# Performance work log

Measured on AMD Instinct MI355X. Metric: run time of the kernel, lower is better.

## Reference

```python
import jax, jax.numpy as jnp
import numpy as np

EPS = 1e-12


def _l2norm(x, axis):
    return x / jnp.maximum(jnp.linalg.norm(x, axis=axis, keepdims=True), EPS)


def _wn_weight(v, g):
    # weight norm over input axis (kernel_size=1): W = g * v / ||v||
    return g * v / jnp.maximum(jnp.linalg.norm(v, axis=0, keepdims=True), EPS)


def setup_inputs() -> dict:
    key = jax.random.key(0)
    ks = jax.random.split(key, 8)
    B, T, D = 16, 4096, 512
    N, K, d = 9, 1024, 8
    return {
        "z": jax.random.normal(ks[0], (B, T, D), dtype=jnp.float32),
        "in_v": jax.random.normal(ks[1], (N, D, d), dtype=jnp.float32) * 0.05,
        "in_g": jax.random.uniform(ks[2], (N, d), dtype=jnp.float32) + 0.5,
        "in_b": jax.random.normal(ks[3], (N, d), dtype=jnp.float32) * 0.01,
        "out_v": jax.random.normal(ks[4], (N, d, D), dtype=jnp.float32) * 0.05,
        "out_g": jax.random.uniform(ks[5], (N, D), dtype=jnp.float32) + 0.5,
        "out_b": jax.random.normal(ks[6], (N, D), dtype=jnp.float32) * 0.01,
        "codebooks": jax.random.normal(ks[7], (N, K, d), dtype=jnp.float32),
    }


def reference(z, in_v, in_g, in_b, out_v, out_g, out_b, codebooks):
    # Eval-mode ResidualVectorQuantize: n_quantizers = n_codebooks, mask all True.
    n_codebooks = codebooks.shape[0]
    residual = z
    z_q = jnp.zeros_like(z)
    commitment_loss = jnp.zeros((), z.dtype)
    codebook_loss = jnp.zeros((), z.dtype)
    codes, latents = [], []
    for i in range(n_codebooks):
        # in_proj (weight-normalized 1x1 conv == linear): [B,T,D] -> [B,T,d]
        W_in = _wn_weight(in_v[i], in_g[i])
        z_e = jnp.einsum("btd,dc->btc", residual, W_in) + in_b[i]
        # decode_latents: l2-normalize, pairwise sq-dist, nearest neighbor
        cb = codebooks[i]                      # [K, d] raw codebook
        enc_n = _l2norm(z_e, axis=-1)          # [B, T, d]
        cb_n = _l2norm(cb, axis=-1)            # [K, d]
        dist = (jnp.sum(enc_n * enc_n, -1, keepdims=True)
                - 2.0 * jnp.einsum("btc,kc->btk", enc_n, cb_n)
                + jnp.sum(cb_n * cb_n, -1))    # [B, T, K]
        indices = jnp.argmax(-dist, axis=-1)   # [B, T]
        z_q_i = cb[indices]                    # gather from raw codebook [B,T,d]
        # per-batch losses (mean over T, d)
        commit_i = jnp.mean((z_e - jax.lax.stop_gradient(z_q_i)) ** 2, axis=(1, 2))
        cbloss_i = jnp.mean((z_q_i - jax.lax.stop_gradient(z_e)) ** 2, axis=(1, 2))
        # straight-through estimator
        z_q_st = z_e + jax.lax.stop_gradient(z_q_i - z_e)
        # out_proj: [B,T,d] -> [B,T,D]
        W_out = _wn_weight(out_v[i], out_g[i])
        z_q_proj = jnp.einsum("btc,cd->btd", z_q_st, W_out) + out_b[i]
        z_q = z_q + z_q_proj
        residual = residual - z_q_proj
        commitment_loss = commitment_loss + commit_i.mean()
        codebook_loss = codebook_loss + cbloss_i.mean()
        codes.append(indices)
        latents.append(z_e)
    codes = jnp.stack(codes, axis=2)           # [B, T, N]
    latents = jnp.concatenate(latents, axis=2) # [B, T, N*d]
    return z_q, codes, latents, commitment_loss, codebook_loss
```

## Files before the change

### kernel.cpp

```cpp
#include <hip/hip_runtime.h>
#include <math.h>

#define ROWS   65536

#define WS_WPAD 0
#define WS_WOUT 49152
#define WS_CBT  86016
#define WS_SC   159744
#define WS_M    168960
#define WS_CACC 174144
#define WS_SOB  174216
#define WS_LOSS 174728

#define OUT_CODES 33554432
#define OUT_LAT   34144256
#define OUT_CLOSS 38862848
#define OUT_CBLOSS 38862849

__device__ __forceinline__ int pcol(int cc){ return (cc/9)*12 + (cc%9); }

__global__ __launch_bounds__(256) void prep1(const float* __restrict__ in_v,
    const float* __restrict__ in_g, const float* __restrict__ out_v,
    const float* __restrict__ out_g, const float* __restrict__ out_b,
    const float* __restrict__ cb, float* __restrict__ ws)
{
    int t = blockIdx.x*256 + threadIdx.x;
    if (t < 9216) {
        int i = t >> 10, k = t & 1023;
        const float* p = cb + (i*1024 + k)*8;
        float v[8]; float ssq = 0.f;
        #pragma unroll
        for (int c=0;c<8;c++){ v[c]=p[c]; ssq = fmaf(v[c],v[c],ssq); }
        float den = fmaxf(sqrtf(ssq), 1e-12f);
        float sc = 0.f;
        #pragma unroll
        for (int c=0;c<8;c++){ float cn = v[c]/den; ws[WS_CBT + (i*8+c)*1024 + k] = cn; sc = fmaf(cn,cn,sc); }
        ws[WS_SC + i*1024 + k] = sc;
    } else if (t < 13824) {
        int r = t - 9216; int j = r >> 9, tt = r & 511;
        float v[8]; float ssq = 0.f;
        #pragma unroll
        for (int a=0;a<8;a++){ v[a]=out_v[(j*8+a)*512+tt]; ssq=fmaf(v[a],v[a],ssq); }
        float den = fmaxf(sqrtf(ssq), 1e-12f);
        float g = out_g[j*512+tt];
        #pragma unroll
        for (int a=0;a<8;a++) ws[WS_WOUT + (j*8+a)*512 + tt] = g*v[a]/den;
    } else if (t < 18432) {
        int r = t - 13824;
        int w = r >> 6, l = r & 63;
        int i = w >> 3, c = w & 7;
        float v[8]; float ssq = 0.f;
        #pragma unroll
        for (int u=0;u<8;u++){ v[u] = in_v[(i*512 + l*8+u)*8 + c]; ssq = fmaf(v[u],v[u],ssq); }
        #pragma unroll
        for (int off=1; off<64; off<<=1) ssq += __shfl_xor(ssq, off, 64);
        float den = fmaxf(sqrtf(ssq), 1e-12f);
        float g = in_g[i*8+c];
        int pc = pcol(i*8+c);
        #pragma unroll
        for (int u=0;u<8;u++) ws[WS_WPAD + (l*8+u)*96 + pc] = g*v[u]/den;
    } else if (t < 18944) {
        int tt = t - 18432;
        float s = 0.f;
        for (int j=0;j<9;j++) s += out_b[j*512+tt];
        ws[WS_SOB + tt] = s;
    } else if (t == 18944) {
        *(double*)&ws[WS_LOSS] = 0.0;
    }
}

__global__ __launch_bounds__(256) void prep2(const float* __restrict__ out_b,
                                             float* __restrict__ ws)
{
    int g = blockIdx.x*256 + threadIdx.x;
    if (g < 41472) {
        int oi = g >> 3, part = g & 7;
        int j = oi / 576; int rem = oi % 576; int i = rem >> 6; int ab = rem & 63;
        int a = ab >> 3, b = ab & 7;
        int pc = pcol(i*8+b);
        const float* wo = ws + WS_WOUT + (j*8+a)*512 + part*64;
        const float* wp = ws + WS_WPAD + (part*64)*96 + pc;
        float s = 0.f;
        #pragma unroll
        for (int u=0; u<16; u++) {
            float4 w4 = *(const float4*)(wo + u*4);
            s = fmaf(w4.x, wp[(u*4+0)*96], s);
            s = fmaf(w4.y, wp[(u*4+1)*96], s);
            s = fmaf(w4.z, wp[(u*4+2)*96], s);
            s = fmaf(w4.w, wp[(u*4+3)*96], s);
        }
        #pragma unroll
        for (int off=1; off<8; off<<=1) s += __shfl_xor(s, off, 64);
        if (part == 0) ws[WS_M + oi] = s;
    } else if (g < 42048) {
        int r = g - 41472;
        int oi = r >> 3, part = r & 7;
        int i = oi >> 3, b = oi & 7;
        int pc = pcol(i*8+b);
        float s = 0.f;
        for (int u=0; u<64; u++) {
            int tt = part*64 + u;
            float bb = 0.f;
            for (int j=0;j<i;j++) bb += out_b[j*512+tt];
            s = fmaf(bb, ws[WS_WPAD + tt*96+pc], s);
        }
        #pragma unroll
        for (int off=1; off<8; off<<=1) s += __shfl_xor(s, off, 64);
        if (part == 0) ws[WS_CACC + oi] = s;
    }
}

__global__ __launch_bounds__(256) void gemm_in(const float* __restrict__ z,
    const float* __restrict__ in_b, const float* __restrict__ ws, float* __restrict__ out)
{
    __shared__ float AsT[32*132];
    __shared__ float Bs[32*96];
    int tid = threadIdx.x;
    int rowbase = blockIdx.x * 128;
    int tr = tid & 31, tc = tid >> 5;
    float acc[4][9];
    #pragma unroll
    for (int r=0;r<4;r++){
        #pragma unroll
        for(int c=0;c<9;c++) acc[r][c]=0.f;
    }
    int kq = tid & 7, rr = tid >> 3;
    for (int kk=0; kk<16; kk++) {
        #pragma unroll
        for (int p=0;p<4;p++){
            int row = rr + p*32;
            float4 a = *(const float4*)(z + (size_t)(rowbase+row)*512 + kk*32 + kq*4);
            AsT[(kq*4+0)*132 + row] = a.x;
            AsT[(kq*4+1)*132 + row] = a.y;
            AsT[(kq*4+2)*132 + row] = a.z;
            AsT[(kq*4+3)*132 + row] = a.w;
        }
        #pragma unroll
        for (int p=0;p<3;p++){
            int idx = p*256 + tid;
            *(float4*)(Bs + idx*4) = *(const float4*)(ws + WS_WPAD + kk*32*96 + idx*4);
        }
        __syncthreads();
        #pragma unroll 4
        for (int k=0;k<32;k++){
            float4 a  = *(const float4*)(AsT + k*132 + tr*4);
            float4 b0 = *(const float4*)(Bs + k*96 + tc*12);
            float4 b1 = *(const float4*)(Bs + k*96 + tc*12 + 4);
            float  b8 = Bs[k*96 + tc*12 + 8];
            float av[4] = {a.x,a.y,a.z,a.w};
            float bv[9] = {b0.x,b0.y,b0.z,b0.w,b1.x,b1.y,b1.z,b1.w,b8};
            #pragma unroll
            for (int r=0;r<4;r++){
                #pragma unroll
                for (int c=0;c<9;c++) acc[r][c] = fmaf(av[r], bv[c], acc[r][c]);
            }
        }
        __syncthreads();
    }
    #pragma unroll
    for (int c=0;c<9;c++){
        int cc = tc*9+c;
        float bias = in_b[cc];
        #pragma unroll
        for (int r=0;r<4;r++){
            int row = rowbase + tr*4 + r;
            out[OUT_LAT + (size_t)row*72 + cc] = acc[r][c] + bias;
        }
    }
}

__global__ __launch_bounds__(256) void step_all(
    const float* __restrict__ cbooks, float* __restrict__ ws, float* __restrict__ out)
{
    __shared__ float lds_cb[8*1056];
    __shared__ float lds_sc[8*132];
    __shared__ float codes_lds[128*13];
    __shared__ float warr[4];

    int tid = threadIdx.x;
    int oct = tid & 7;
    int rowslot = tid >> 3;
    int rowbase = blockIdx.x * 128;
    const int kbase = oct*128;
    const float* cbo = lds_cb + oct*132;
    const float* sco = lds_sc + oct*132;

    float lacc = 0.f;

    for (int i=0; i<9; i++){
        __syncthreads();
        #pragma unroll
        for (int p=0;p<8;p++){
            int s = (p*256 + tid)*4;
            int c = s >> 10; int k = s & 1023; int o = k >> 7; int kk = k & 127;
            float4 v = *(const float4*)(ws + WS_CBT + i*8192 + s);
            *(float4*)(lds_cb + c*1056 + o*132 + kk) = v;
        }
        {
            int s = tid*4;
            int o = s >> 7; int kk = s & 127;
            float4 v = *(const float4*)(ws + WS_SC + i*1024 + s);
            v.x *= 0.5f; v.y *= 0.5f; v.z *= 0.5f; v.w *= 0.5f;
            *(float4*)(lds_sc + o*132 + kk) = v;
        }
        __syncthreads();

        float zen[4][8];
        #pragma unroll
        for (int r=0;r<4;r++){
            int rib = r*32 + rowslot;
            int row = rowbase + rib;
            float* lat = out + OUT_LAT + (size_t)row*72 + i*8;
            float4 p0 = *(const float4*)(lat);
            float4 p1 = *(const float4*)(lat+4);
            float ze[8] = {p0.x,p0.y,p0.z,p0.w,p1.x,p1.y,p1.z,p1.w};
            #pragma unroll
            for (int b=0;b<8;b++) ze[b] -= ws[WS_CACC + i*8 + b];
            for (int j=0;j<i;j++){
                int kj = (int)codes_lds[rib*13 + j];
                const float* qp = cbooks + (size_t)(j*1024+kj)*8;
                float4 q0 = *(const float4*)(qp);
                float4 q1 = *(const float4*)(qp+4);
                float qa[8] = {q0.x,q0.y,q0.z,q0.w,q1.x,q1.y,q1.z,q1.w};
                const float* M = ws + WS_M + (j*9+i)*64;
                #pragma unroll
                for (int a=0;a<8;a++){
                    #pragma unroll
                    for (int b=0;b<8;b++) ze[b] = fmaf(-qa[a], M[a*8+b], ze[b]);
                }
            }
            float ssq = 0.f;
            #pragma unroll
            for (int c=0;c<8;c++) ssq = fmaf(ze[c],ze[c],ssq);
            float den = fmaxf(sqrtf(ssq), 1e-12f);
            float rden = 1.0f/den;
            if (oct == 0){
                float4 z0 = {ze[0],ze[1],ze[2],ze[3]};
                float4 z1 = {ze[4],ze[5],ze[6],ze[7]};
                *(float4*)(lat)   = z0;
                *(float4*)(lat+4) = z1;
            }
            #pragma unroll
            for (int c=0;c<8;c++) zen[r][c] = ze[c]*rden;
        }

        float bv[4]; int bk[4];
        #pragma unroll
        for (int r=0;r<4;r++){ bv[r] = -3.0e38f; bk[r] = kbase; }
        #pragma unroll 2
        for (int kk=0; kk<128; kk+=4){
            float4 v[8];
            #pragma unroll
            for (int c=0;c<8;c++) v[c] = *(const float4*)(cbo + c*1056 + kk);
            float4 hs = *(const float4*)(sco + kk);
            #pragma unroll
            for (int r=0;r<4;r++){
                float d0=0.f,d1=0.f,d2=0.f,d3=0.f;
                #pragma unroll
                for (int c=0;c<8;c++){
                    d0 = fmaf(zen[r][c], v[c].x, d0);
                    d1 = fmaf(zen[r][c], v[c].y, d1);
                    d2 = fmaf(zen[r][c], v[c].z, d2);
                    d3 = fmaf(zen[r][c], v[c].w, d3);
                }
                float t0 = d0 - hs.x;
                float t1 = d1 - hs.y;
                float t2 = d2 - hs.z;
                float t3 = d3 - hs.w;
                bool c0 = t0 > bv[r]; bk[r] = c0?(kbase+kk+0):bk[r]; bv[r] = c0?t0:bv[r];
                bool c1 = t1 > bv[r]; bk[r] = c1?(kbase+kk+1):bk[r]; bv[r] = c1?t1:bv[r];
                bool c2 = t2 > bv[r]; bk[r] = c2?(kbase+kk+2):bk[r]; bv[r] = c2?t2:bv[r];
                bool c3 = t3 > bv[r]; bk[r] = c3?(kbase+kk+3):bk[r]; bv[r] = c3?t3:bv[r];
            }
        }

        #pragma unroll
        for (int off=1; off<8; off<<=1){
            #pragma unroll
            for (int r=0;r<4;r++){
                float ov = __shfl_xor(bv[r], off, 64);
                int   ok = __shfl_xor(bk[r], off, 64);
                bool rep = (ov > bv[r]) || (ov == bv[r] && ok < bk[r]);
                bv[r] = rep ? ov : bv[r];
                bk[r] = rep ? ok : bk[r];
            }
        }
        if (oct == 0){
            #pragma unroll
            for (int r=0;r<4;r++){
                int rib = r*32 + rowslot;
                int row = rowbase + rib;
                out[OUT_CODES + (size_t)row*9 + i] = (float)bk[r];
                codes_lds[rib*13 + i] = (float)bk[r];
                const float* lat = out + OUT_LAT + (size_t)row*72 + i*8;
                const float* qp = cbooks + (size_t)(i*1024+bk[r])*8;
                float4 z0 = *(const float4*)(lat);
                float4 z1 = *(const float4*)(lat+4);
                float4 q0 = *(const float4*)(qp);
                float4 q1 = *(const float4*)(qp+4);
                float e0 = z0.x-q0.x, e1 = z0.y-q0.y, e2 = z0.z-q0.z, e3 = z0.w-q0.w;
                float e4 = z1.x-q1.x, e5 = z1.y-q1.y, e6 = z1.z-q1.z, e7 = z1.w-q1.w;
                lacc = fmaf(e0,e0,lacc); lacc = fmaf(e1,e1,lacc);
                lacc = fmaf(e2,e2,lacc); lacc = fmaf(e3,e3,lacc);
                lacc = fmaf(e4,e4,lacc); lacc = fmaf(e5,e5,lacc);
                lacc = fmaf(e6,e6,lacc); lacc = fmaf(e7,e7,lacc);
            }
        }
    }

    #pragma unroll
    for (int off=1; off<64; off<<=1) lacc += __shfl_xor(lacc, off, 64);
    if ((tid & 63)==0) warr[tid>>6] = lacc;
    __syncthreads();
    if (tid==0){
        double bs = (double)warr[0]+(double)warr[1]+(double)warr[2]+(double)warr[3];
        atomicAdd((double*)&ws[WS_LOSS], bs);
    }
}

__global__ __launch_bounds__(256) void gemm_out(const float* __restrict__ cbooks,
    const float* __restrict__ ws, float* __restrict__ out)
{
    __shared__ float QL[64*76];
    __shared__ float Ws[72*128];
    int tid = threadIdx.x;
    int rowbase = blockIdx.x*64;
    if (tid < 64){
        int row = rowbase + tid;
        for (int j=0;j<9;j++){
            int kj = (int)out[OUT_CODES + (size_t)row*9 + j];
            const float* qp = cbooks + (j*1024+kj)*8;
            float4 q0 = *(const float4*)qp;
            float4 q1 = *(const float4*)(qp+4);
            *(float4*)(QL + tid*76 + j*8)     = q0;
            *(float4*)(QL + tid*76 + j*8 + 4) = q1;
        }
    }
    int tr = tid & 15, tc = tid >> 4;
    for (int cc=0; cc<4; cc++){
        __syncthreads();
        #pragma unroll
        for (int p=0;p<9;p++){
            int idx = p*256 + tid;
            int jr = idx >> 5; int cq = idx & 31;
            *(float4*)(Ws + jr*128 + cq*4) = *(const float4*)(ws + WS_WOUT + jr*512 + cc*128 + cq*4);
        }
        __syncthreads();
        float acc[4][8];
        #pragma unroll
        for (int r=0;r<4;r++){
            #pragma unroll
            for (int c=0;c<8;c++) acc[r][c]=0.f;
        }
        #pragma unroll 4
        for (int k=0;k<72;k++){
            float a0 = QL[(tr*4+0)*76 + k];
            float a1 = QL[(tr*4+1)*76 + k];
            float a2 = QL[(tr*4+2)*76 + k];
            float a3 = QL[(tr*4+3)*76 + k];
            float4 b0 = *(const float4*)(Ws + k*128 + tc*8);
            float4 b1 = *(const float4*)(Ws + k*128 + tc*8 + 4);
            float bv[8] = {b0.x,b0.y,b0.z,b0.w,b1.x,b1.y,b1.z,b1.w};
            float av[4] = {a0,a1,a2,a3};
            #pragma unroll
            for (int r=0;r<4;r++){
                #pragma unroll
                for (int c=0;c<8;c++) acc[r][c] = fmaf(av[r], bv[c], acc[r][c]);
            }
        }
        float4 s0 = *(const float4*)(ws + WS_SOB + cc*128 + tc*8);
        float4 s1 = *(const float4*)(ws + WS_SOB + cc*128 + tc*8 + 4);
        #pragma unroll
        for (int r=0;r<4;r++){
            int row = rowbase + tr*4 + r;
            float4 o0 = {acc[r][0]+s0.x, acc[r][1]+s0.y, acc[r][2]+s0.z, acc[r][3]+s0.w};
            float4 o1 = {acc[r][4]+s1.x, acc[r][5]+s1.y, acc[r][6]+s1.z, acc[r][7]+s1.w};
            *(float4*)(out + (size_t)row*512 + cc*128 + tc*8)     = o0;
            *(float4*)(out + (size_t)row*512 + cc*128 + tc*8 + 4) = o1;
        }
    }
    if (blockIdx.x==0 && tid==0){
        double L = *(const double*)(ws + WS_LOSS);
        float lv = (float)(L * (1.0/524288.0));
        out[OUT_CLOSS]  = lv;
        out[OUT_CBLOSS] = lv;
    }
}

extern "C" void kernel_launch(void* const* d_in, const int* in_sizes, int n_in,
                              void* d_out, int out_size, void* d_ws, size_t ws_size,
                              hipStream_t stream) {
    const float* z     = (const float*)d_in[0];
    const float* in_v  = (const float*)d_in[1];
    const float* in_g  = (const float*)d_in[2];
    const float* in_b  = (const float*)d_in[3];
    const float* out_v = (const float*)d_in[4];
    const float* out_g = (const float*)d_in[5];
    const float* out_b = (const float*)d_in[6];
    const float* cb    = (const float*)d_in[7];
    float* out = (float*)d_out;
    float* ws  = (float*)d_ws;

    prep1<<<75, 256, 0, stream>>>(in_v, in_g, out_v, out_g, out_b, cb, ws);
    prep2<<<165, 256, 0, stream>>>(out_b, ws);
    gemm_in<<<512, 256, 0, stream>>>(z, in_b, ws, out);
    step_all<<<512, 256, 0, stream>>>(cb, ws, out);
    gemm_out<<<1024, 256, 0, stream>>>(cb, ws, out);
}
```

Measured before the change: 660.4 us.

## Widen step_all to 512 threads and retile gemm_out to 8x8 transposed tiles

Measured after the change: 677.2 us. 2.5% more time.

```diff
diff --git a/kernel.cpp b/kernel.cpp
--- a/kernel.cpp
+++ b/kernel.cpp
@@ -169,13 +169,13 @@
     }
 }
 
-__global__ __launch_bounds__(256) void step_all(
+__global__ __launch_bounds__(512, 4) void step_all(
     const float* __restrict__ cbooks, float* __restrict__ ws, float* __restrict__ out)
 {
     __shared__ float lds_cb[8*1056];
     __shared__ float lds_sc[8*132];
     __shared__ float codes_lds[128*13];
-    __shared__ float warr[4];
+    __shared__ float warr[8];
 
     int tid = threadIdx.x;
     int oct = tid & 7;
@@ -190,13 +190,13 @@
     for (int i=0; i<9; i++){
         __syncthreads();
         #pragma unroll
-        for (int p=0;p<8;p++){
-            int s = (p*256 + tid)*4;
+        for (int p=0;p<4;p++){
+            int s = (p*512 + tid)*4;
             int c = s >> 10; int k = s & 1023; int o = k >> 7; int kk = k & 127;
             float4 v = *(const float4*)(ws + WS_CBT + i*8192 + s);
             *(float4*)(lds_cb + c*1056 + o*132 + kk) = v;
         }
-        {
+        if (tid < 256){
             int s = tid*4;
             int o = s >> 7; int kk = s & 127;
             float4 v = *(const float4*)(ws + WS_SC + i*1024 + s);
@@ -205,10 +205,10 @@
         }
         __syncthreads();
 
-        float zen[4][8];
-        #pragma unroll
-        for (int r=0;r<4;r++){
-            int rib = r*32 + rowslot;
+        float zen[2][8];
+        #pragma unroll
+        for (int r=0;r<2;r++){
+            int rib = r*64 + rowslot;
             int row = rowbase + rib;
             float* lat = out + OUT_LAT + (size_t)row*72 + i*8;
             float4 p0 = *(const float4*)(lat);
@@ -244,9 +244,9 @@
             for (int c=0;c<8;c++) zen[r][c] = ze[c]*rden;
         }
 
-        float bv[4]; int bk[4];
-        #pragma unroll
-        for (int r=0;r<4;r++){ bv[r] = -3.0e38f; bk[r] = kbase; }
+        float bv[2]; int bk[2];
+        #pragma unroll
+        for (int r=0;r<2;r++){ bv[r] = -3.0e38f; bk[r] = kbase; }
         #pragma unroll 2
         for (int kk=0; kk<128; kk+=4){
             float4 v[8];
@@ -254,8 +254,8 @@
             for (int c=0;c<8;c++) v[c] = *(const float4*)(cbo + c*1056 + kk);
             float4 hs = *(const float4*)(sco + kk);
             #pragma unroll
-            for (int r=0;r<4;r++){
-                float d0=0.f,d1=0.f,d2=0.f,d3=0.f;
+            for (int r=0;r<2;r++){
+                float d0=-hs.x, d1=-hs.y, d2=-hs.z, d3=-hs.w;
                 #pragma unroll
                 for (int c=0;c<8;c++){
                     d0 = fmaf(zen[r][c], v[c].x, d0);
@@ -263,21 +263,17 @@
                     d2 = fmaf(zen[r][c], v[c].z, d2);
                     d3 = fmaf(zen[r][c], v[c].w, d3);
                 }
-                float t0 = d0 - hs.x;
-                float t1 = d1 - hs.y;
-                float t2 = d2 - hs.z;
-                float t3 = d3 - hs.w;
-                bool c0 = t0 > bv[r]; bk[r] = c0?(kbase+kk+0):bk[r]; bv[r] = c0?t0:bv[r];
-                bool c1 = t1 > bv[r]; bk[r] = c1?(kbase+kk+1):bk[r]; bv[r] = c1?t1:bv[r];
-                bool c2 = t2 > bv[r]; bk[r] = c2?(kbase+kk+2):bk[r]; bv[r] = c2?t2:bv[r];
-                bool c3 = t3 > bv[r]; bk[r] = c3?(kbase+kk+3):bk[r]; bv[r] = c3?t3:bv[r];
+                bool c0 = d0 > bv[r]; bk[r] = c0?(kbase+kk+0):bk[r]; bv[r] = c0?d0:bv[r];
+                bool c1 = d1 > bv[r]; bk[r] = c1?(kbase+kk+1):bk[r]; bv[r] = c1?d1:bv[r];
+                bool c2 = d2 > bv[r]; bk[r] = c2?(kbase+kk+2):bk[r]; bv[r] = c2?d2:bv[r];
+                bool c3 = d3 > bv[r]; bk[r] = c3?(kbase+kk+3):bk[r]; bv[r] = c3?d3:bv[r];
             }
         }
 
         #pragma unroll
         for (int off=1; off<8; off<<=1){
             #pragma unroll
-            for (int r=0;r<4;r++){
+            for (int r=0;r<2;r++){
                 float ov = __shfl_xor(bv[r], off, 64);
                 int   ok = __shfl_xor(bk[r], off, 64);
                 bool rep = (ov > bv[r]) || (ov == bv[r] && ok < bk[r]);
@@ -287,8 +283,8 @@
         }
         if (oct == 0){
             #pragma unroll
-            for (int r=0;r<4;r++){
-                int rib = r*32 + rowslot;
+            for (int r=0;r<2;r++){
+                int rib = r*64 + rowslot;
                 int row = rowbase + rib;
                 out[OUT_CODES + (size_t)row*9 + i] = (float)bk[r];
                 codes_lds[rib*13 + i] = (float)bk[r];
@@ -313,7 +309,9 @@
     if ((tid & 63)==0) warr[tid>>6] = lacc;
     __syncthreads();
     if (tid==0){
-        double bs = (double)warr[0]+(double)warr[1]+(double)warr[2]+(double)warr[3];
+        double bs = 0.0;
+        #pragma unroll
+        for (int w=0; w<8; w++) bs += (double)warr[w];
         atomicAdd((double*)&ws[WS_LOSS], bs);
     }
 }
@@ -321,58 +319,66 @@
 __global__ __launch_bounds__(256) void gemm_out(const float* __restrict__ cbooks,
     const float* __restrict__ ws, float* __restrict__ out)
 {
-    __shared__ float QL[64*76];
-    __shared__ float Ws[72*128];
+    __shared__ float QLT[72*140];
+    __shared__ float Ws[72*140];
     int tid = threadIdx.x;
-    int rowbase = blockIdx.x*64;
-    if (tid < 64){
+    int rowbase = blockIdx.x*128;
+    if (tid < 128){
         int row = rowbase + tid;
+        int rsw = tid + (tid>>5)*4;
         for (int j=0;j<9;j++){
             int kj = (int)out[OUT_CODES + (size_t)row*9 + j];
-            const float* qp = cbooks + (j*1024+kj)*8;
+            const float* qp = cbooks + (size_t)(j*1024+kj)*8;
             float4 q0 = *(const float4*)qp;
             float4 q1 = *(const float4*)(qp+4);
-            *(float4*)(QL + tid*76 + j*8)     = q0;
-            *(float4*)(QL + tid*76 + j*8 + 4) = q1;
-        }
-    }
-    int tr = tid & 15, tc = tid >> 4;
+            QLT[(j*8+0)*140 + rsw] = q0.x;
+            QLT[(j*8+1)*140 + rsw] = q0.y;
+            QLT[(j*8+2)*140 + rsw] = q0.z;
+            QLT[(j*8+3)*140 + rsw] = q0.w;
+            QLT[(j*8+4)*140 + rsw] = q1.x;
+            QLT[(j*8+5)*140 + rsw] = q1.y;
+            QLT[(j*8+6)*140 + rsw] = q1.z;
+            QLT[(j*8+7)*140 + rsw] = q1.w;
+        }
+    }
+    int tc = tid & 15, tr = tid >> 4;
+    int aoff = tr*8 + (tr>>2)*4;
+    int boff = tc*8 + (tc>>2)*4;
     for (int cc=0; cc<4; cc++){
         __syncthreads();
         #pragma unroll
         for (int p=0;p<9;p++){
             int idx = p*256 + tid;
             int jr = idx >> 5; int cq = idx & 31;
-            *(float4*)(Ws + jr*128 + cq*4) = *(const float4*)(ws + WS_WOUT + jr*512 + cc*128 + cq*4);
-        }
-        __syncthreads();
-        float acc[4][8];
-        #pragma unroll
-        for (int r=0;r<4;r++){
+            float4 w = *(const float4*)(ws + WS_WOUT + jr*512 + cc*128 + cq*4);
+            *(float4*)(Ws + jr*140 + cq*4 + (cq>>3)*4) = w;
+        }
+        __syncthreads();
+        float acc[8][8];
+        #pragma unroll
+        for (int r=0;r<8;r++){
             #pragma unroll
             for (int c=0;c<8;c++) acc[r][c]=0.f;
         }
-        #pragma unroll 4
+        #pragma unroll 2
         for (int k=0;k<72;k++){
-            float a0 = QL[(tr*4+0)*76 + k];
-            float a1 = QL[(tr*4+1)*76 + k];
-            float a2 = QL[(tr*4+2)*76 + k];
-            float a3 = QL[(tr*4+3)*76 + k];
-            float4 b0 = *(const float4*)(Ws + k*128 + tc*8);
-            float4 b1 = *(const float4*)(Ws + k*128 + tc*8 + 4);
-            float bv[8] = {b0.x,b0.y,b0.z,b0.w,b1.x,b1.y,b1.z,b1.w};
-            float av[4] = {a0,a1,a2,a3};
-            #pragma unroll
-            for (int r=0;r<4;r++){
+            float4 a0 = *(const float4*)(QLT + k*140 + aoff);
+            float4 a1 = *(const float4*)(QLT + k*140 + aoff + 4);
+            float4 b0 = *(const float4*)(Ws + k*140 + boff);
+            float4 b1 = *(const float4*)(Ws + k*140 + boff + 4);
+            float av[8] = {a0.x,a0.y,a0.z,a0.w,a1.x,a1.y,a1.z,a1.w};
+            float bw[8] = {b0.x,b0.y,b0.z,b0.w,b1.x,b1.y,b1.z,b1.w};
+            #pragma unroll
+            for (int r=0;r<8;r++){
                 #pragma unroll
-                for (int c=0;c<8;c++) acc[r][c] = fmaf(av[r], bv[c], acc[r][c]);
+                for (int c=0;c<8;c++) acc[r][c] = fmaf(av[r], bw[c], acc[r][c]);
             }
         }
         float4 s0 = *(const float4*)(ws + WS_SOB + cc*128 + tc*8);
         float4 s1 = *(const float4*)(ws + WS_SOB + cc*128 + tc*8 + 4);
         #pragma unroll
-        for (int r=0;r<4;r++){
-            int row = rowbase + tr*4 + r;
+        for (int r=0;r<8;r++){
+            int row = rowbase + tr*8 + r;
             float4 o0 = {acc[r][0]+s0.x, acc[r][1]+s0.y, acc[r][2]+s0.z, acc[r][3]+s0.w};
             float4 o1 = {acc[r][4]+s1.x, acc[r][5]+s1.y, acc[r][6]+s1.z, acc[r][7]+s1.w};
             *(float4*)(out + (size_t)row*512 + cc*128 + tc*8)     = o0;
@@ -404,6 +410,6 @@
     prep1<<<75, 256, 0, stream>>>(in_v, in_g, out_v, out_g, out_b, cb, ws);
     prep2<<<165, 256, 0, stream>>>(out_b, ws);
     gemm_in<<<512, 256, 0, stream>>>(z, in_b, ws, out);
-    step_all<<<512, 256, 0, stream>>>(cb, ws, out);
-    gemm_out<<<1024, 256, 0, stream>>>(cb, ws, out);
-}
+    step_all<<<512, 512, 0, stream>>>(cb, ws, out);
+    gemm_out<<<512, 256, 0, stream>>>(cb, ws, out);
+}
```
